# Optimization experiments

Measured on AMD Instinct MI355X. Metric: run time of the kernel, lower is better.

Reference implementation:

```python
import jax, jax.numpy as jnp
import numpy as np

B, T, HID, H = 2, 2048, 2048, 16
D = HID // H  # 128


def apply_rope(x):
    # Faithful port of the torch helper: treats x dims as (B, T, H, D)
    # regardless of the caller's actual layout (this reproduces the
    # original module's quirk of rotating q along the head axis).
    b, t, h, d = x.shape
    half = d // 2
    x1, x2 = x[..., :half], x[..., half:]
    theta = 1.0 / (10000.0 ** (jnp.arange(0, half, 2, dtype=jnp.float32) / half))
    pos = jnp.arange(t, dtype=jnp.float32)
    freq = pos[:, None] * theta[None, :]            # (t, half//2)
    sin = jnp.sin(freq)[None, :, None, :]
    cos = jnp.cos(freq)[None, :, None, :]
    x1e, x1o = x1[..., ::2], x1[..., 1::2]
    x2e, x2o = x2[..., ::2], x2[..., 1::2]
    x1r = jnp.concatenate([x1e * cos - x1o * sin, x1e * sin + x1o * cos], axis=-1)
    x2r = jnp.concatenate([x2e * cos - x2o * sin, x2e * sin + x2o * cos], axis=-1)
    return jnp.concatenate([x1r, x2r], axis=-1)


def setup_inputs() -> dict:
    key = jax.random.key(0)
    ks = jax.random.split(key, 5)
    s = 0.02
    return {
        "hidden_states": jax.random.normal(ks[0], (B, T, HID), dtype=jnp.float32),
        "Wq": jax.random.normal(ks[1], (HID, HID), dtype=jnp.float32) * s,
        "Wk": jax.random.normal(ks[2], (D, HID), dtype=jnp.float32) * s,
        "Wv": jax.random.normal(ks[3], (D, HID), dtype=jnp.float32) * s,
        "Wo": jax.random.normal(ks[4], (HID, HID), dtype=jnp.float32) * s,
    }


def reference(hidden_states, Wq, Wk, Wv, Wo):
    b, t, _ = hidden_states.shape
    scaling = D ** -0.5
    # projections (nn.Linear: x @ W.T)
    q = (hidden_states @ Wq.T).reshape(b, t, H, D).transpose(0, 2, 1, 3)  # (B,H,T,D)
    k = hidden_states @ Wk.T                                             # (B,T,D)
    v = hidden_states @ Wv.T                                             # (B,T,D)
    # RoPE applied exactly as in the torch module (note layout quirk)
    q = apply_rope(q)                 # rotated along head axis, as original
    k = apply_rope(k[:, None])        # (B,1,T,D): pos=0 -> permutation only
    v = v[:, None]                    # (B,1,T,D)
    scores = jnp.einsum("bhqd,bokd->bhqk", q, k) * scaling  # (B,H,T,T)
    causal = jnp.tril(jnp.ones((t, t), dtype=bool))
    scores = jnp.where(causal[None, None], scores, -jnp.inf)
    probs = jax.nn.softmax(scores, axis=-1)
    attn = jnp.einsum("bhqk,bokd->bhqd", probs, v)           # (B,H,T,D)
    attn = attn.transpose(0, 2, 1, 3).reshape(b, t, HID)
    return attn @ Wo.T
```

## Files before the change

### kernel.cpp

```cpp
#include <hip/hip_runtime.h>
#include <math.h>


typedef unsigned short u16;
typedef __attribute__((ext_vector_type(8))) short s16x8;
typedef __attribute__((ext_vector_type(4))) float f32x4;

#define B_   2
#define T_   2048
#define HID_ 2048
#define H_   16
#define D_   128

__device__ __forceinline__ u16 f2bf(float f) {
  unsigned u = __float_as_uint(f);
  unsigned r = ((u >> 16) & 1u) + 0x7fffu;
  return (u16)((u + r) >> 16);
}
__device__ __forceinline__ float bf2f(u16 b) {
  return __uint_as_float(((unsigned)b) << 16);
}

__global__ void cast_f32_to_bf16(const float* __restrict__ in,
                                 u16* __restrict__ out, int n4) {
  int i = blockIdx.x * blockDim.x + threadIdx.x;
  if (i >= n4) return;
  float4 v = reinterpret_cast<const float4*>(in)[i];
  ushort4 o;
  o.x = f2bf(v.x); o.y = f2bf(v.y); o.z = f2bf(v.z); o.w = f2bf(v.w);
  reinterpret_cast<ushort4*>(out)[i] = o;
}

__device__ __forceinline__ void gload_lds16(const u16* g, u16* lds) {
  __builtin_amdgcn_global_load_lds(
      (const __attribute__((address_space(1))) void*)g,
      (__attribute__((address_space(3))) void*)lds, 16, 0, 0);
}

template <int OUT_BF16>
__global__ __launch_bounds__(256) void gemm_bt(
    const u16* __restrict__ A, const u16* __restrict__ Bm,
    void* __restrict__ Cv, int M, int N, int K) {
  __shared__ __align__(16) u16 As[128 * 64];
  __shared__ __align__(16) u16 Bs[128 * 64];
  const int tid = threadIdx.x;
  const int w = tid >> 6, l = tid & 63;
  const int bm = blockIdx.x, bn = blockIdx.y;
  const int wm = (w >> 1) * 64, wn = (w & 1) * 64;
  const int lg = l >> 4, lc = l & 15;
  const int srow = l >> 3, slot = l & 7;
  f32x4 acc[4][4] = {};

  for (int k0 = 0; k0 < K; k0 += 64) {
#pragma unroll
    for (int i = 0; i < 4; ++i) {
      int R = (w * 4 + i) * 8;
      int row = R + srow;
      int c = slot ^ (row & 7);
      gload_lds16(A + (size_t)(bm * 128 + row) * K + k0 + c * 8, &As[R * 64]);
      gload_lds16(Bm + (size_t)(bn * 128 + row) * K + k0 + c * 8, &Bs[R * 64]);
    }
    __syncthreads();
#pragma unroll
    for (int kc = 0; kc < 2; ++kc) {
      s16x8 af[4], bfv[4];
#pragma unroll
      for (int mi = 0; mi < 4; ++mi) {
        int r = wm + mi * 16 + lc;
        int cc = kc * 4 + lg;
        af[mi] = *(const s16x8*)((const char*)As + r * 128 + ((cc ^ (r & 7)) * 16));
      }
#pragma unroll
      for (int ni = 0; ni < 4; ++ni) {
        int r = wn + ni * 16 + lc;
        int cc = kc * 4 + lg;
        bfv[ni] = *(const s16x8*)((const char*)Bs + r * 128 + ((cc ^ (r & 7)) * 16));
      }
#pragma unroll
      for (int mi = 0; mi < 4; ++mi)
#pragma unroll
        for (int ni = 0; ni < 4; ++ni)
          acc[mi][ni] = __builtin_amdgcn_mfma_f32_16x16x32_bf16(
              af[mi], bfv[ni], acc[mi][ni], 0, 0, 0);
    }
    __syncthreads();
  }
#pragma unroll
  for (int mi = 0; mi < 4; ++mi)
#pragma unroll
    for (int ni = 0; ni < 4; ++ni) {
      int mrow = bm * 128 + wm + mi * 16 + lg * 4;
      int ncol = bn * 128 + wn + ni * 16 + lc;
#pragma unroll
      for (int r = 0; r < 4; ++r) {
        float v = acc[mi][ni][r];
        if (OUT_BF16)
          ((u16*)Cv)[(size_t)(mrow + r) * N + ncol] = f2bf(v);
        else
          ((float*)Cv)[(size_t)(mrow + r) * N + ncol] = v;
      }
    }
}

__global__ void rope_q(u16* __restrict__ Q) {
  int idx = blockIdx.x * blockDim.x + threadIdx.x;
  int row = idx >> 10;
  int p = idx & 1023;
  int h = p >> 6;
  int i = p & 63;
  int j = i & 31;
  int d = (i < 32) ? (2 * i) : (64 + 2 * (i - 32));
  float theta = exp2f(-(float)j * (13.287712379549449f / 32.0f));
  float ang = (float)h * theta;
  float s, c;
  __sincosf(ang, &s, &c);
  unsigned* pq = (unsigned*)(Q + (size_t)row * HID_ + h * D_ + d);
  unsigned v = *pq;
  float a = bf2f((u16)(v & 0xffffu));
  float b = bf2f((u16)(v >> 16));
  *pq = ((unsigned)f2bf(a * s + b * c) << 16) | (unsigned)f2bf(a * c - b * s);
}

__global__ void transpose_v(const u16* __restrict__ V, u16* __restrict__ Vt) {
  int idx = blockIdx.x * blockDim.x + threadIdx.x;
  int t = idx & (T_ - 1);
  int d = (idx >> 11) & (D_ - 1);
  int b = idx >> 18;
  Vt[idx] = V[(size_t)(b * T_ + t) * D_ + d];
}

__global__ __launch_bounds__(256, 2) void mqa_attn(
    const u16* __restrict__ Q, const u16* __restrict__ K,
    const u16* __restrict__ Vt, u16* __restrict__ O) {
  __shared__ __align__(16) u16 Plds[4][2][16][136];
  const int tid = threadIdx.x;
  const int w = tid >> 6, l = tid & 63;
  const int lg = l >> 4, lc = l & 15;
  const int idx = blockIdx.x * 4 + w;
  const int h = blockIdx.y, b = blockIdx.z;
  const int ga = idx, gb = 127 - idx;
  const int q0a = ga * 16, q0b = gb * 16;
  const int nka = ga / 8 + 1, nkb = gb / 8 + 1;
  const u16* Kp = K + (size_t)b * T_ * D_;
  const u16* Vb = Vt + (size_t)b * D_ * T_;

  s16x8 qfa[4], qfb[4];
  {
    const u16* qa = Q + (size_t)(b * T_ + q0a + lc) * HID_ + h * D_ + lg * 8;
    const u16* qb = Q + (size_t)(b * T_ + q0b + lc) * HID_ + h * D_ + lg * 8;
#pragma unroll
    for (int kc = 0; kc < 4; ++kc) {
      qfa[kc] = *(const s16x8*)(qa + kc * 32);
      qfb[kc] = *(const s16x8*)(qb + kc * 32);
    }
  }

  float lA[4] = {0.f, 0.f, 0.f, 0.f}, lB[4] = {0.f, 0.f, 0.f, 0.f};
  f32x4 accA[8] = {}, accB[8] = {};
  const float scale = 0.08838834764831845f;

  for (int kt = 0; kt < nkb; ++kt) {
    const int kb = kt * 128;
    const bool doA = (kt < nka);
    const bool lastA = (kt == nka - 1);
    const bool lastB = (kt == nkb - 1);
    s16x8 vf0[8];
#pragma unroll
    for (int dt = 0; dt < 8; ++dt)
      vf0[dt] = *(const s16x8*)(Vb + (size_t)(dt * 16 + lc) * T_ + kb + lg * 8);
#pragma unroll
    for (int s = 0; s < 8; ++s) {
      const u16* kp = Kp + (size_t)(kb + s * 16 + lc) * D_ + lg * 8;
      s16x8 kf0 = *(const s16x8*)(kp);
      s16x8 kf1 = *(const s16x8*)(kp + 32);
      s16x8 kf2 = *(const s16x8*)(kp + 64);
      s16x8 kf3 = *(const s16x8*)(kp + 96);
      const int kcol = kb + s * 16 + lc;
      __builtin_amdgcn_s_setprio(1);
      f32x4 aB = {0.f, 0.f, 0.f, 0.f};
      aB = __builtin_amdgcn_mfma_f32_16x16x32_bf16(qfb[0], kf0, aB, 0, 0, 0);
      aB = __builtin_amdgcn_mfma_f32_16x16x32_bf16(qfb[1], kf1, aB, 0, 0, 0);
      aB = __builtin_amdgcn_mfma_f32_16x16x32_bf16(qfb[2], kf2, aB, 0, 0, 0);
      aB = __builtin_amdgcn_mfma_f32_16x16x32_bf16(qfb[3], kf3, aB, 0, 0, 0);
      __builtin_amdgcn_s_setprio(0);
#pragma unroll
      for (int r = 0; r < 4; ++r) {
        float x = fminf(aB[r] * scale, 30.f);
        if (lastB && (kcol > q0b + lg * 4 + r)) x = -INFINITY;
        float pp = __expf(x);
        lB[r] += pp;
        Plds[w][1][lg * 4 + r][s * 16 + lc] = f2bf(pp);
      }
      if (doA) {
        __builtin_amdgcn_s_setprio(1);
        f32x4 aA = {0.f, 0.f, 0.f, 0.f};
        aA = __builtin_amdgcn_mfma_f32_16x16x32_bf16(qfa[0], kf0, aA, 0, 0, 0);
        aA = __builtin_amdgcn_mfma_f32_16x16x32_bf16(qfa[1], kf1, aA, 0, 0, 0);
        aA = __builtin_amdgcn_mfma_f32_16x16x32_bf16(qfa[2], kf2, aA, 0, 0, 0);
        aA = __builtin_amdgcn_mfma_f32_16x16x32_bf16(qfa[3], kf3, aA, 0, 0, 0);
        __builtin_amdgcn_s_setprio(0);
#pragma unroll
        for (int r = 0; r < 4; ++r) {
          float x = fminf(aA[r] * scale, 30.f);
          if (lastA && (kcol > q0a + lg * 4 + r)) x = -INFINITY;
          float pp = __expf(x);
          lA[r] += pp;
          Plds[w][0][lg * 4 + r][s * 16 + lc] = f2bf(pp);
        }
      }
    }
#pragma unroll
    for (int ph = 0; ph < 4; ++ph) {
      s16x8 paB = *(const s16x8*)&Plds[w][1][lc][ph * 32 + lg * 8];
      __builtin_amdgcn_s_setprio(1);
      if (doA) {
        s16x8 paA = *(const s16x8*)&Plds[w][0][lc][ph * 32 + lg * 8];
#pragma unroll
        for (int dt = 0; dt < 8; ++dt) {
          s16x8 vf = (ph == 0) ? vf0[dt]
                   : *(const s16x8*)(Vb + (size_t)(dt * 16 + lc) * T_ + kb + ph * 32 + lg * 8);
          accB[dt] = __builtin_amdgcn_mfma_f32_16x16x32_bf16(paB, vf, accB[dt], 0, 0, 0);
          accA[dt] = __builtin_amdgcn_mfma_f32_16x16x32_bf16(paA, vf, accA[dt], 0, 0, 0);
        }
      } else {
#pragma unroll
        for (int dt = 0; dt < 8; ++dt) {
          s16x8 vf = (ph == 0) ? vf0[dt]
                   : *(const s16x8*)(Vb + (size_t)(dt * 16 + lc) * T_ + kb + ph * 32 + lg * 8);
          accB[dt] = __builtin_amdgcn_mfma_f32_16x16x32_bf16(paB, vf, accB[dt], 0, 0, 0);
        }
      }
      __builtin_amdgcn_s_setprio(0);
    }
  }
#pragma unroll
  for (int m = 1; m < 16; m <<= 1)
#pragma unroll
    for (int r = 0; r < 4; ++r) {
      lA[r] += __shfl_xor(lA[r], m, 64);
      lB[r] += __shfl_xor(lB[r], m, 64);
    }
  u16* oa = O + (size_t)(b * T_ + q0a + lg * 4) * HID_ + h * D_ + lc;
  u16* ob = O + (size_t)(b * T_ + q0b + lg * 4) * HID_ + h * D_ + lc;
#pragma unroll
  for (int dt = 0; dt < 8; ++dt)
#pragma unroll
    for (int r = 0; r < 4; ++r) {
      oa[(size_t)r * HID_ + dt * 16] = f2bf(accA[dt][r] / lA[r]);
      ob[(size_t)r * HID_ + dt * 16] = f2bf(accB[dt][r] / lB[r]);
    }
}

extern "C" void kernel_launch(void* const* d_in, const int* in_sizes, int n_in,
                              void* d_out, int out_size, void* d_ws, size_t ws_size,
                              hipStream_t stream) {
  const float* hs = (const float*)d_in[0];
  const float* Wq = (const float*)d_in[1];
  const float* Wk = (const float*)d_in[2];
  const float* Wv = (const float*)d_in[3];
  const float* Wo = (const float*)d_in[4];
  float* out = (float*)d_out;
  char* ws = (char*)d_ws;

  u16* hb  = (u16*)(ws + 0);
  u16* wqb = (u16*)(ws + 16777216);
  u16* wkb = (u16*)(ws + 25165824);
  u16* wvb = (u16*)(ws + 25690112);
  u16* wob = (u16*)(ws + 26214400);
  u16* Qb  = (u16*)(ws + 34603008);
  u16* Kb  = (u16*)(ws + 51380224);
  u16* Vb  = (u16*)(ws + 52428800);
  u16* Vtb = (u16*)(ws + 53477376);
  u16* Ab  = (u16*)(ws + 54525952);

  cast_f32_to_bf16<<<8192, 256, 0, stream>>>(hs, hb, 2097152);
  cast_f32_to_bf16<<<4096, 256, 0, stream>>>(Wq, wqb, 1048576);
  cast_f32_to_bf16<<<256, 256, 0, stream>>>(Wk, wkb, 65536);
  cast_f32_to_bf16<<<256, 256, 0, stream>>>(Wv, wvb, 65536);
  cast_f32_to_bf16<<<4096, 256, 0, stream>>>(Wo, wob, 1048576);

  gemm_bt<1><<<dim3(32, 16), 256, 0, stream>>>(hb, wqb, Qb, 4096, 2048, 2048);
  gemm_bt<1><<<dim3(32, 1), 256, 0, stream>>>(hb, wkb, Kb, 4096, 128, 2048);
  gemm_bt<1><<<dim3(32, 1), 256, 0, stream>>>(hb, wvb, Vb, 4096, 128, 2048);

  rope_q<<<16384, 256, 0, stream>>>(Qb);
  transpose_v<<<2048, 256, 0, stream>>>(Vb, Vtb);

  mqa_attn<<<dim3(16, 16, 2), 256, 0, stream>>>(Qb, Kb, Vtb, Ab);

  gemm_bt<0><<<dim3(32, 16), 256, 0, stream>>>(Ab, wob, out, 4096, 2048, 2048);

  (void)in_sizes; (void)n_in; (void)out_size; (void)ws_size;
}
```

Baseline: 428.9 us.

## Split attention KV range across wave pairs with LDS reduction of partial outputs

```diff
diff --git a/kernel.cpp b/kernel.cpp
--- a/kernel.cpp
+++ b/kernel.cpp
@@ -129,18 +129,20 @@
   Vt[idx] = V[(size_t)(b * T_ + t) * D_ + d];
 }
 
-__global__ __launch_bounds__(256, 2) void mqa_attn(
+__global__ __launch_bounds__(512, 4) void mqa_attn(
     const u16* __restrict__ Q, const u16* __restrict__ K,
     const u16* __restrict__ Vt, u16* __restrict__ O) {
-  __shared__ __align__(16) u16 Plds[4][2][16][136];
+  __shared__ __align__(16) u16 Plds[8][2][16][72];
+  __shared__ float Lbuf[4][2][16];
   const int tid = threadIdx.x;
   const int w = tid >> 6, l = tid & 63;
   const int lg = l >> 4, lc = l & 15;
-  const int idx = blockIdx.x * 4 + w;
+  const int wp = w >> 1, sp = w & 1;
+  const int idx = blockIdx.x * 4 + wp;
   const int h = blockIdx.y, b = blockIdx.z;
   const int ga = idx, gb = 127 - idx;
   const int q0a = ga * 16, q0b = gb * 16;
-  const int nka = ga / 8 + 1, nkb = gb / 8 + 1;
+  const int nka = ga / 4 + 1, nkb = gb / 4 + 1;
   const u16* Kp = K + (size_t)b * T_ * D_;
   const u16* Vb = Vt + (size_t)b * D_ * T_;
 
@@ -159,8 +161,8 @@
   f32x4 accA[8] = {}, accB[8] = {};
   const float scale = 0.08838834764831845f;
 
-  for (int kt = 0; kt < nkb; ++kt) {
-    const int kb = kt * 128;
+  for (int kt = sp; kt < nkb; kt += 2) {
+    const int kb = kt * 64;
     const bool doA = (kt < nka);
     const bool lastA = (kt == nka - 1);
     const bool lastB = (kt == nkb - 1);
@@ -169,7 +171,7 @@
     for (int dt = 0; dt < 8; ++dt)
       vf0[dt] = *(const s16x8*)(Vb + (size_t)(dt * 16 + lc) * T_ + kb + lg * 8);
 #pragma unroll
-    for (int s = 0; s < 8; ++s) {
+    for (int s = 0; s < 4; ++s) {
       const u16* kp = Kp + (size_t)(kb + s * 16 + lc) * D_ + lg * 8;
       s16x8 kf0 = *(const s16x8*)(kp);
       s16x8 kf1 = *(const s16x8*)(kp + 32);
@@ -210,7 +212,7 @@
       }
     }
 #pragma unroll
-    for (int ph = 0; ph < 4; ++ph) {
+    for (int ph = 0; ph < 2; ++ph) {
       s16x8 paB = *(const s16x8*)&Plds[w][1][lc][ph * 32 + lg * 8];
       __builtin_amdgcn_s_setprio(1);
       if (doA) {
@@ -218,7 +220,7 @@
 #pragma unroll
         for (int dt = 0; dt < 8; ++dt) {
           s16x8 vf = (ph == 0) ? vf0[dt]
-                   : *(const s16x8*)(Vb + (size_t)(dt * 16 + lc) * T_ + kb + ph * 32 + lg * 8);
+                   : *(const s16x8*)(Vb + (size_t)(dt * 16 + lc) * T_ + kb + 32 + lg * 8);
           accB[dt] = __builtin_amdgcn_mfma_f32_16x16x32_bf16(paB, vf, accB[dt], 0, 0, 0);
           accA[dt] = __builtin_amdgcn_mfma_f32_16x16x32_bf16(paA, vf, accA[dt], 0, 0, 0);
         }
@@ -226,7 +228,7 @@
 #pragma unroll
         for (int dt = 0; dt < 8; ++dt) {
           s16x8 vf = (ph == 0) ? vf0[dt]
-                   : *(const s16x8*)(Vb + (size_t)(dt * 16 + lc) * T_ + kb + ph * 32 + lg * 8);
+                   : *(const s16x8*)(Vb + (size_t)(dt * 16 + lc) * T_ + kb + 32 + lg * 8);
           accB[dt] = __builtin_amdgcn_mfma_f32_16x16x32_bf16(paB, vf, accB[dt], 0, 0, 0);
         }
       }
@@ -240,15 +242,43 @@
       lA[r] += __shfl_xor(lA[r], m, 64);
       lB[r] += __shfl_xor(lB[r], m, 64);
     }
-  u16* oa = O + (size_t)(b * T_ + q0a + lg * 4) * HID_ + h * D_ + lc;
-  u16* ob = O + (size_t)(b * T_ + q0b + lg * 4) * HID_ + h * D_ + lc;
-#pragma unroll
-  for (int dt = 0; dt < 8; ++dt)
+  __syncthreads();
+  u16* mb = &Plds[0][0][0][0];
+  if (sp) {
+#pragma unroll
+    for (int dt = 0; dt < 8; ++dt)
+#pragma unroll
+      for (int r = 0; r < 4; ++r) {
+        mb[(size_t)((wp * 2 + 0) * 16 + lg * 4 + r) * 128 + dt * 16 + lc] = f2bf(accA[dt][r]);
+        mb[(size_t)((wp * 2 + 1) * 16 + lg * 4 + r) * 128 + dt * 16 + lc] = f2bf(accB[dt][r]);
+      }
+    if (lc == 0) {
+#pragma unroll
+      for (int r = 0; r < 4; ++r) {
+        Lbuf[wp][0][lg * 4 + r] = lA[r];
+        Lbuf[wp][1][lg * 4 + r] = lB[r];
+      }
+    }
+  }
+  __syncthreads();
+  if (!sp) {
 #pragma unroll
     for (int r = 0; r < 4; ++r) {
-      oa[(size_t)r * HID_ + dt * 16] = f2bf(accA[dt][r] / lA[r]);
-      ob[(size_t)r * HID_ + dt * 16] = f2bf(accB[dt][r] / lB[r]);
-    }
+      lA[r] += Lbuf[wp][0][lg * 4 + r];
+      lB[r] += Lbuf[wp][1][lg * 4 + r];
+    }
+    u16* oa = O + (size_t)(b * T_ + q0a + lg * 4) * HID_ + h * D_ + lc;
+    u16* ob = O + (size_t)(b * T_ + q0b + lg * 4) * HID_ + h * D_ + lc;
+#pragma unroll
+    for (int dt = 0; dt < 8; ++dt)
+#pragma unroll
+      for (int r = 0; r < 4; ++r) {
+        float va = accA[dt][r] + bf2f(mb[(size_t)((wp * 2 + 0) * 16 + lg * 4 + r) * 128 + dt * 16 + lc]);
+        float vb = accB[dt][r] + bf2f(mb[(size_t)((wp * 2 + 1) * 16 + lg * 4 + r) * 128 + dt * 16 + lc]);
+        oa[(size_t)r * HID_ + dt * 16] = f2bf(va / lA[r]);
+        ob[(size_t)r * HID_ + dt * 16] = f2bf(vb / lB[r]);
+      }
+  }
 }
 
 extern "C" void kernel_launch(void* const* d_in, const int* in_sizes, int n_in,
@@ -286,7 +316,7 @@
   rope_q<<<16384, 256, 0, stream>>>(Qb);
   transpose_v<<<2048, 256, 0, stream>>>(Vb, Vtb);
 
-  mqa_attn<<<dim3(16, 16, 2), 256, 0, stream>>>(Qb, Kb, Vtb, Ab);
+  mqa_attn<<<dim3(16, 16, 2), 512, 0, stream>>>(Qb, Kb, Vtb, Ab);
 
   gemm_bt<0><<<dim3(32, 16), 256, 0, stream>>>(Ab, wob, out, 4096, 2048, 2048);
 
```

Result: slower. 699.7 us (+63.1%).

## Halve attention key tile and register-prefetch next K tile across iterations

Applied to the files above, without the earlier changes.

```diff
diff --git a/kernel.cpp b/kernel.cpp
--- a/kernel.cpp
+++ b/kernel.cpp
@@ -132,7 +132,7 @@
 __global__ __launch_bounds__(256, 2) void mqa_attn(
     const u16* __restrict__ Q, const u16* __restrict__ K,
     const u16* __restrict__ Vt, u16* __restrict__ O) {
-  __shared__ __align__(16) u16 Plds[4][2][16][136];
+  __shared__ __align__(16) u16 Plds[4][2][16][72];
   const int tid = threadIdx.x;
   const int w = tid >> 6, l = tid & 63;
   const int lg = l >> 4, lc = l & 15;
@@ -140,7 +140,7 @@
   const int h = blockIdx.y, b = blockIdx.z;
   const int ga = idx, gb = 127 - idx;
   const int q0a = ga * 16, q0b = gb * 16;
-  const int nka = ga / 8 + 1, nkb = gb / 8 + 1;
+  const int nka = ga / 4 + 1, nkb = gb / 4 + 1;
   const u16* Kp = K + (size_t)b * T_ * D_;
   const u16* Vb = Vt + (size_t)b * D_ * T_;
 
@@ -159,30 +159,46 @@
   f32x4 accA[8] = {}, accB[8] = {};
   const float scale = 0.08838834764831845f;
 
+  s16x8 kpre[4][4];
+#pragma unroll
+  for (int s = 0; s < 4; ++s) {
+    const u16* kp = Kp + (size_t)(s * 16 + lc) * D_ + lg * 8;
+#pragma unroll
+    for (int kc = 0; kc < 4; ++kc) kpre[s][kc] = *(const s16x8*)(kp + kc * 32);
+  }
+
   for (int kt = 0; kt < nkb; ++kt) {
-    const int kb = kt * 128;
+    const int kb = kt * 64;
     const bool doA = (kt < nka);
     const bool lastA = (kt == nka - 1);
     const bool lastB = (kt == nkb - 1);
+    const bool more = (kt + 1 < nkb);
     s16x8 vf0[8];
 #pragma unroll
     for (int dt = 0; dt < 8; ++dt)
       vf0[dt] = *(const s16x8*)(Vb + (size_t)(dt * 16 + lc) * T_ + kb + lg * 8);
 #pragma unroll
-    for (int s = 0; s < 8; ++s) {
-      const u16* kp = Kp + (size_t)(kb + s * 16 + lc) * D_ + lg * 8;
-      s16x8 kf0 = *(const s16x8*)(kp);
-      s16x8 kf1 = *(const s16x8*)(kp + 32);
-      s16x8 kf2 = *(const s16x8*)(kp + 64);
-      s16x8 kf3 = *(const s16x8*)(kp + 96);
+    for (int s = 0; s < 4; ++s) {
       const int kcol = kb + s * 16 + lc;
       __builtin_amdgcn_s_setprio(1);
       f32x4 aB = {0.f, 0.f, 0.f, 0.f};
-      aB = __builtin_amdgcn_mfma_f32_16x16x32_bf16(qfb[0], kf0, aB, 0, 0, 0);
-      aB = __builtin_amdgcn_mfma_f32_16x16x32_bf16(qfb[1], kf1, aB, 0, 0, 0);
-      aB = __builtin_amdgcn_mfma_f32_16x16x32_bf16(qfb[2], kf2, aB, 0, 0, 0);
-      aB = __builtin_amdgcn_mfma_f32_16x16x32_bf16(qfb[3], kf3, aB, 0, 0, 0);
+      aB = __builtin_amdgcn_mfma_f32_16x16x32_bf16(qfb[0], kpre[s][0], aB, 0, 0, 0);
+      aB = __builtin_amdgcn_mfma_f32_16x16x32_bf16(qfb[1], kpre[s][1], aB, 0, 0, 0);
+      aB = __builtin_amdgcn_mfma_f32_16x16x32_bf16(qfb[2], kpre[s][2], aB, 0, 0, 0);
+      aB = __builtin_amdgcn_mfma_f32_16x16x32_bf16(qfb[3], kpre[s][3], aB, 0, 0, 0);
+      f32x4 aA = {0.f, 0.f, 0.f, 0.f};
+      if (doA) {
+        aA = __builtin_amdgcn_mfma_f32_16x16x32_bf16(qfa[0], kpre[s][0], aA, 0, 0, 0);
+        aA = __builtin_amdgcn_mfma_f32_16x16x32_bf16(qfa[1], kpre[s][1], aA, 0, 0, 0);
+        aA = __builtin_amdgcn_mfma_f32_16x16x32_bf16(qfa[2], kpre[s][2], aA, 0, 0, 0);
+        aA = __builtin_amdgcn_mfma_f32_16x16x32_bf16(qfa[3], kpre[s][3], aA, 0, 0, 0);
+      }
       __builtin_amdgcn_s_setprio(0);
+      if (more) {
+        const u16* kp = Kp + (size_t)(kb + 64 + s * 16 + lc) * D_ + lg * 8;
+#pragma unroll
+        for (int kc = 0; kc < 4; ++kc) kpre[s][kc] = *(const s16x8*)(kp + kc * 32);
+      }
 #pragma unroll
       for (int r = 0; r < 4; ++r) {
         float x = fminf(aB[r] * scale, 30.f);
@@ -192,13 +208,6 @@
         Plds[w][1][lg * 4 + r][s * 16 + lc] = f2bf(pp);
       }
       if (doA) {
-        __builtin_amdgcn_s_setprio(1);
-        f32x4 aA = {0.f, 0.f, 0.f, 0.f};
-        aA = __builtin_amdgcn_mfma_f32_16x16x32_bf16(qfa[0], kf0, aA, 0, 0, 0);
-        aA = __builtin_amdgcn_mfma_f32_16x16x32_bf16(qfa[1], kf1, aA, 0, 0, 0);
-        aA = __builtin_amdgcn_mfma_f32_16x16x32_bf16(qfa[2], kf2, aA, 0, 0, 0);
-        aA = __builtin_amdgcn_mfma_f32_16x16x32_bf16(qfa[3], kf3, aA, 0, 0, 0);
-        __builtin_amdgcn_s_setprio(0);
 #pragma unroll
         for (int r = 0; r < 4; ++r) {
           float x = fminf(aA[r] * scale, 30.f);
@@ -210,7 +219,7 @@
       }
     }
 #pragma unroll
-    for (int ph = 0; ph < 4; ++ph) {
+    for (int ph = 0; ph < 2; ++ph) {
       s16x8 paB = *(const s16x8*)&Plds[w][1][lc][ph * 32 + lg * 8];
       __builtin_amdgcn_s_setprio(1);
       if (doA) {
@@ -218,7 +227,7 @@
 #pragma unroll
         for (int dt = 0; dt < 8; ++dt) {
           s16x8 vf = (ph == 0) ? vf0[dt]
-                   : *(const s16x8*)(Vb + (size_t)(dt * 16 + lc) * T_ + kb + ph * 32 + lg * 8);
+                   : *(const s16x8*)(Vb + (size_t)(dt * 16 + lc) * T_ + kb + 32 + lg * 8);
           accB[dt] = __builtin_amdgcn_mfma_f32_16x16x32_bf16(paB, vf, accB[dt], 0, 0, 0);
           accA[dt] = __builtin_amdgcn_mfma_f32_16x16x32_bf16(paA, vf, accA[dt], 0, 0, 0);
         }
@@ -226,7 +235,7 @@
 #pragma unroll
         for (int dt = 0; dt < 8; ++dt) {
           s16x8 vf = (ph == 0) ? vf0[dt]
-                   : *(const s16x8*)(Vb + (size_t)(dt * 16 + lc) * T_ + kb + ph * 32 + lg * 8);
+                   : *(const s16x8*)(Vb + (size_t)(dt * 16 + lc) * T_ + kb + 32 + lg * 8);
           accB[dt] = __builtin_amdgcn_mfma_f32_16x16x32_bf16(paB, vf, accB[dt], 0, 0, 0);
         }
       }
```

New measurement: 553.4 us. 29.0% more time.

## Split causal attention over key halves with a separate merge kernel

Applied to the files above, without the earlier changes.

```diff
diff --git a/kernel.cpp b/kernel.cpp
--- a/kernel.cpp
+++ b/kernel.cpp
@@ -129,10 +129,121 @@
   Vt[idx] = V[(size_t)(b * T_ + t) * D_ + d];
 }
 
+__global__ __launch_bounds__(256, 3) void mqa_attn_split(
+    const u16* __restrict__ Q, const u16* __restrict__ K,
+    const u16* __restrict__ Vt, u16* __restrict__ Opart,
+    float* __restrict__ Lpart) {
+  __shared__ __align__(16) u16 Plds[4][16][72];
+  const int tid = threadIdx.x;
+  const int w = tid >> 6, l = tid & 63;
+  const int lg = l >> 4, lc = l & 15;
+  const int t = blockIdx.x >> 1, seg = blockIdx.x & 1;
+  const int h = blockIdx.y, b = blockIdx.z;
+  const int g = t * 4 + w;
+  const int q0 = g * 16;
+  const int n = t + 1;
+  const int h0 = (n + 1) >> 1;
+  const int klo = seg ? h0 : 0, khi = seg ? n : h0;
+  const u16* Kp = K + (size_t)b * T_ * D_;
+  const u16* Vb = Vt + (size_t)b * D_ * T_;
+
+  s16x8 qf[4];
+  const u16* qbase = Q + (size_t)(b * T_ + q0 + lc) * HID_ + h * D_ + lg * 8;
+#pragma unroll
+  for (int kc = 0; kc < 4; ++kc) qf[kc] = *(const s16x8*)(qbase + kc * 32);
+
+  float ls[4] = {0.f, 0.f, 0.f, 0.f};
+  f32x4 acc[8] = {};
+  const float scale = 0.08838834764831845f;
+
+  for (int kt = klo; kt < khi; ++kt) {
+    const int kb = kt * 64;
+    const bool lastc = (kt == n - 1);
+    s16x8 vf0[8];
+#pragma unroll
+    for (int dt = 0; dt < 8; ++dt)
+      vf0[dt] = *(const s16x8*)(Vb + (size_t)(dt * 16 + lc) * T_ + kb + lg * 8);
+#pragma unroll
+    for (int s = 0; s < 4; ++s) {
+      const u16* kp = Kp + (size_t)(kb + s * 16 + lc) * D_ + lg * 8;
+      s16x8 kf0 = *(const s16x8*)(kp);
+      s16x8 kf1 = *(const s16x8*)(kp + 32);
+      s16x8 kf2 = *(const s16x8*)(kp + 64);
+      s16x8 kf3 = *(const s16x8*)(kp + 96);
+      const int kcol = kb + s * 16 + lc;
+      __builtin_amdgcn_s_setprio(1);
+      f32x4 a = {0.f, 0.f, 0.f, 0.f};
+      a = __builtin_amdgcn_mfma_f32_16x16x32_bf16(qf[0], kf0, a, 0, 0, 0);
+      a = __builtin_amdgcn_mfma_f32_16x16x32_bf16(qf[1], kf1, a, 0, 0, 0);
+      a = __builtin_amdgcn_mfma_f32_16x16x32_bf16(qf[2], kf2, a, 0, 0, 0);
+      a = __builtin_amdgcn_mfma_f32_16x16x32_bf16(qf[3], kf3, a, 0, 0, 0);
+      __builtin_amdgcn_s_setprio(0);
+#pragma unroll
+      for (int r = 0; r < 4; ++r) {
+        float x = fminf(a[r] * scale, 30.f);
+        if (lastc && (kcol > q0 + lg * 4 + r)) x = -INFINITY;
+        float pp = __expf(x);
+        ls[r] += pp;
+        Plds[w][lg * 4 + r][s * 16 + lc] = f2bf(pp);
+      }
+    }
+#pragma unroll
+    for (int ph = 0; ph < 2; ++ph) {
+      s16x8 pa = *(const s16x8*)&Plds[w][lc][ph * 32 + lg * 8];
+      __builtin_amdgcn_s_setprio(1);
+#pragma unroll
+      for (int dt = 0; dt < 8; ++dt) {
+        s16x8 vf = (ph == 0) ? vf0[dt]
+                 : *(const s16x8*)(Vb + (size_t)(dt * 16 + lc) * T_ + kb + 32 + lg * 8);
+        acc[dt] = __builtin_amdgcn_mfma_f32_16x16x32_bf16(pa, vf, acc[dt], 0, 0, 0);
+      }
+      __builtin_amdgcn_s_setprio(0);
+    }
+  }
+#pragma unroll
+  for (int m = 1; m < 16; m <<= 1)
+#pragma unroll
+    for (int r = 0; r < 4; ++r)
+      ls[r] += __shfl_xor(ls[r], m, 64);
+  const int job = (((b * 16 + h) * 128 + g) * 2 + seg);
+  u16* op = Opart + (size_t)job * 2048 + (lg * 4) * 128 + lc;
+#pragma unroll
+  for (int dt = 0; dt < 8; ++dt)
+#pragma unroll
+    for (int r = 0; r < 4; ++r)
+      op[r * 128 + dt * 16] = f2bf(acc[dt][r]);
+  if (lc == 0) {
+#pragma unroll
+    for (int r = 0; r < 4; ++r)
+      Lpart[job * 16 + lg * 4 + r] = ls[r];
+  }
+}
+
+__global__ void merge_attn(const u16* __restrict__ Opart,
+                           const float* __restrict__ Lpart,
+                           u16* __restrict__ Ab) {
+  int idx = blockIdx.x * blockDim.x + threadIdx.x;
+  int cg = idx & 15;
+  int row = (idx >> 4) & 15;
+  int jobm = idx >> 8;
+  int g = jobm & 127, h = (jobm >> 7) & 15, b = jobm >> 11;
+  size_t p0 = ((size_t)jobm * 2) * 2048 + row * 128 + cg * 8;
+  float l0 = Lpart[(jobm * 2) * 16 + row];
+  float l1 = Lpart[(jobm * 2 + 1) * 16 + row];
+  float linv = 1.f / (l0 + l1);
+  s16x8 a = *(const s16x8*)(Opart + p0);
+  s16x8 c = *(const s16x8*)(Opart + p0 + 2048);
+  s16x8 o;
+#pragma unroll
+  for (int j = 0; j < 8; ++j)
+    o[j] = (short)f2bf((bf2f((u16)a[j]) + bf2f((u16)c[j])) * linv);
+  *(s16x8*)(Ab + (size_t)(b * T_ + g * 16 + row) * HID_ + h * 128 + cg * 8) = o;
+}
+
 __global__ __launch_bounds__(256, 2) void mqa_attn(
     const u16* __restrict__ Q, const u16* __restrict__ K,
     const u16* __restrict__ Vt, u16* __restrict__ O) {
-  __shared__ __align__(16) u16 Plds[4][2][16][136];
+  __shared__ __align__(16) u16 Plds[4][2][16][72];
   const int tid = threadIdx.x;
   const int w = tid >> 6, l = tid & 63;
   const int lg = l >> 4, lc = l & 15;
@@ -140,7 +251,7 @@
   const int h = blockIdx.y, b = blockIdx.z;
   const int ga = idx, gb = 127 - idx;
   const int q0a = ga * 16, q0b = gb * 16;
-  const int nka = ga / 8 + 1, nkb = gb / 8 + 1;
+  const int nka = ga / 4 + 1, nkb = gb / 4 + 1;
   const u16* Kp = K + (size_t)b * T_ * D_;
   const u16* Vb = Vt + (size_t)b * D_ * T_;
 
@@ -154,13 +265,12 @@
       qfb[kc] = *(const s16x8*)(qb + kc * 32);
     }
   }
-
   float lA[4] = {0.f, 0.f, 0.f, 0.f}, lB[4] = {0.f, 0.f, 0.f, 0.f};
   f32x4 accA[8] = {}, accB[8] = {};
   const float scale = 0.08838834764831845f;
 
   for (int kt = 0; kt < nkb; ++kt) {
-    const int kb = kt * 128;
+    const int kb = kt * 64;
     const bool doA = (kt < nka);
     const bool lastA = (kt == nka - 1);
     const bool lastB = (kt == nkb - 1);
@@ -169,7 +279,7 @@
     for (int dt = 0; dt < 8; ++dt)
       vf0[dt] = *(const s16x8*)(Vb + (size_t)(dt * 16 + lc) * T_ + kb + lg * 8);
 #pragma unroll
-    for (int s = 0; s < 8; ++s) {
+    for (int s = 0; s < 4; ++s) {
       const u16* kp = Kp + (size_t)(kb + s * 16 + lc) * D_ + lg * 8;
       s16x8 kf0 = *(const s16x8*)(kp);
       s16x8 kf1 = *(const s16x8*)(kp + 32);
@@ -210,7 +320,7 @@
       }
     }
 #pragma unroll
-    for (int ph = 0; ph < 4; ++ph) {
+    for (int ph = 0; ph < 2; ++ph) {
       s16x8 paB = *(const s16x8*)&Plds[w][1][lc][ph * 32 + lg * 8];
       __builtin_amdgcn_s_setprio(1);
       if (doA) {
@@ -218,7 +328,7 @@
 #pragma unroll
         for (int dt = 0; dt < 8; ++dt) {
           s16x8 vf = (ph == 0) ? vf0[dt]
-                   : *(const s16x8*)(Vb + (size_t)(dt * 16 + lc) * T_ + kb + ph * 32 + lg * 8);
+                   : *(const s16x8*)(Vb + (size_t)(dt * 16 + lc) * T_ + kb + 32 + lg * 8);
           accB[dt] = __builtin_amdgcn_mfma_f32_16x16x32_bf16(paB, vf, accB[dt], 0, 0, 0);
           accA[dt] = __builtin_amdgcn_mfma_f32_16x16x32_bf16(paA, vf, accA[dt], 0, 0, 0);
         }
@@ -226,7 +336,7 @@
 #pragma unroll
         for (int dt = 0; dt < 8; ++dt) {
           s16x8 vf = (ph == 0) ? vf0[dt]
-                   : *(const s16x8*)(Vb + (size_t)(dt * 16 + lc) * T_ + kb + ph * 32 + lg * 8);
+                   : *(const s16x8*)(Vb + (size_t)(dt * 16 + lc) * T_ + kb + 32 + lg * 8);
           accB[dt] = __builtin_amdgcn_mfma_f32_16x16x32_bf16(paB, vf, accB[dt], 0, 0, 0);
         }
       }
@@ -272,6 +382,8 @@
   u16* Vb  = (u16*)(ws + 52428800);
   u16* Vtb = (u16*)(ws + 53477376);
   u16* Ab  = (u16*)(ws + 54525952);
+  u16* Opart = (u16*)(ws + 71303168);
+  float* Lpart = (float*)(ws + 104857600);
 
   cast_f32_to_bf16<<<8192, 256, 0, stream>>>(hs, hb, 2097152);
   cast_f32_to_bf16<<<4096, 256, 0, stream>>>(Wq, wqb, 1048576);
@@ -286,9 +398,14 @@
   rope_q<<<16384, 256, 0, stream>>>(Qb);
   transpose_v<<<2048, 256, 0, stream>>>(Vb, Vtb);
 
-  mqa_attn<<<dim3(16, 16, 2), 256, 0, stream>>>(Qb, Kb, Vtb, Ab);
+  if (ws_size >= 105381888ULL) {
+    mqa_attn_split<<<dim3(64, 16, 2), 256, 0, stream>>>(Qb, Kb, Vtb, Opart, Lpart);
+    merge_attn<<<4096, 256, 0, stream>>>(Opart, Lpart, Ab);
+  } else {
+    mqa_attn<<<dim3(16, 16, 2), 256, 0, stream>>>(Qb, Kb, Vtb, Ab);
+  }
 
   gemm_bt<0><<<dim3(32, 16), 256, 0, stream>>>(Ab, wob, out, 4096, 2048, 2048);
 
-  (void)in_sizes; (void)n_in; (void)out_size; (void)ws_size;
-}
+  (void)in_sizes; (void)n_in; (void)out_size;
+}
```

Measured after the change: 590.4 us. 37.7% more time.
